# Performance work log

Hardware: AMD Instinct MI355X
Metric: run time of the kernel (lower is better)

Reference implementation:

```python
import jax, jax.numpy as jnp
import numpy as np


def _lstm_encode(x_tbF, W_ih, W_hh, b_ih, b_hh):
    """torch nn.LSTM (single layer), x: [T, B, F]. Returns final (h, c), each [B, H]."""
    H = W_hh.shape[1]
    B = x_tbF.shape[1]
    b = b_ih + b_hh

    def step(carry, xt):
        h, c = carry
        gates = xt @ W_ih.T + h @ W_hh.T + b  # [B, 4H]
        i, f, g, o = jnp.split(gates, 4, axis=-1)
        c = jax.nn.sigmoid(f) * c + jax.nn.sigmoid(i) * jnp.tanh(g)
        h = jax.nn.sigmoid(o) * jnp.tanh(c)
        return (h, c), None

    init = (jnp.zeros((B, H), x_tbF.dtype), jnp.zeros((B, H), x_tbF.dtype))
    (h, c), _ = jax.lax.scan(step, init, x_tbF)
    return h, c


def reference(speed, pos, Ws_ih, Ws_hh, bs_ih, bs_hh, Wp_ih, Wp_hh, bp_ih, bp_hh,
              Wd_ih, Wd_hh, bd_ih, bd_hh, W_fc, b_fc, W_emb, b_emb, seq_len):
    # Encoders consume time-major inputs (module does speed.permute(1,0,2))
    sh, sc = _lstm_encode(jnp.transpose(speed, (1, 0, 2)), Ws_ih, Ws_hh, bs_ih, bs_hh)
    ph, pc = _lstm_encode(jnp.transpose(pos, (1, 0, 2)), Wp_ih, Wp_hh, bp_ih, bp_hh)

    h0 = ph + sh
    c0 = pc + sc
    last_pos0 = pos[:, -1, :]  # [B, 4]
    bd = bd_ih + bd_hh

    def dec_step(carry, _):
        h, c, last_pos = carry
        gates = last_pos @ Wd_ih.T + h @ Wd_hh.T + bd  # [B, 4H]
        i, f, g, o = jnp.split(gates, 4, axis=-1)
        c = jax.nn.sigmoid(f) * c + jax.nn.sigmoid(i) * jnp.tanh(g)
        h = jax.nn.sigmoid(o) * jnp.tanh(c)
        crossing = jax.nn.relu(h @ W_fc.T + b_fc)        # fc_crossing: [B, 2]
        last_pos = jax.nn.relu(crossing @ W_emb.T + b_emb)  # pos_embedding: [B, 4]
        probs = jax.nn.softmax(crossing, axis=1)
        return (h, c, last_pos), probs

    _, probs = jax.lax.scan(dec_step, (h0, c0, last_pos0), None, length=seq_len)
    return jnp.transpose(probs, (1, 0, 2))  # [B, seq_len, 2]


def setup_inputs() -> dict:
    B, T, H, F = 8192, 16, 512, 4
    seq_len = 16
    key = jax.random.key(0)
    ks = jax.random.split(key, 20)
    s = 1.0 / np.sqrt(H)

    def u(k, shape):
        return jax.random.uniform(k, shape, jnp.float32, -s, s)

    return {
        "speed": jax.random.normal(ks[0], (B, T, F), jnp.float32),
        "pos": jax.random.normal(ks[1], (B, T, F), jnp.float32),
        "Ws_ih": u(ks[2], (4 * H, F)), "Ws_hh": u(ks[3], (4 * H, H)),
        "bs_ih": u(ks[4], (4 * H,)), "bs_hh": u(ks[5], (4 * H,)),
        "Wp_ih": u(ks[6], (4 * H, F)), "Wp_hh": u(ks[7], (4 * H, H)),
        "bp_ih": u(ks[8], (4 * H,)), "bp_hh": u(ks[9], (4 * H,)),
        "Wd_ih": u(ks[10], (4 * H, F)), "Wd_hh": u(ks[11], (4 * H, H)),
        "bd_ih": u(ks[12], (4 * H,)), "bd_hh": u(ks[13], (4 * H,)),
        "W_fc": u(ks[14], (2, H)), "b_fc": u(ks[15], (2,)),
        "W_emb": u(ks[16], (4, 2)), "b_emb": u(ks[17], (4,)),
        "seq_len": seq_len,
    }
```

## Files before the change

### kernel.cpp

```cpp
#include <hip/hip_runtime.h>

#define NBLK 256
#define NTHR 512
#define MTILE 32
#define KPADI 592
#define HSTR  528
#define CHB   (9*8*64*16)
#define LSTR  (16*CHB)

typedef __attribute__((ext_vector_type(4))) int int4v;

__device__ inline float ex2(float x){ return __builtin_amdgcn_exp2f(x); }
__device__ inline float rcpf_(float d){ return __builtin_amdgcn_rcpf(d); }
__device__ inline float rcpn(float d){ float r=__builtin_amdgcn_rcpf(d); return r*(2.f-d*r); }
#define LOG2E 1.4426950408889634f
__device__ inline float sigf(float x){ return rcpf_(1.f+ex2(-LOG2E*x)); }
__device__ inline float tanh_(float x){ return 2.f*rcpf_(1.f+ex2(-2.f*LOG2E*x))-1.f; }

__device__ inline void lbar(){
    asm volatile("s_waitcnt lgkmcnt(0)\n\ts_barrier" ::: "memory");
}

__global__ void scale_k(const float* Ws_ih, const float* Ws_hh, const float* bs_ih, const float* bs_hh,
                        const float* Wp_ih, const float* Wp_hh, const float* bp_ih, const float* bp_hh,
                        const float* Wd_ih, const float* Wd_hh, const float* bd_ih, const float* bd_hh,
                        int* smax)
{
    int L = blockIdx.x >> 5;
    int blk = blockIdx.x & 31;
    const float* Wih = L==0 ? Ws_ih : L==1 ? Wp_ih : Wd_ih;
    const float* Whh = L==0 ? Ws_hh : L==1 ? Wp_hh : Wd_hh;
    const float* bih = L==0 ? bs_ih : L==1 ? bp_ih : bd_ih;
    const float* bhh = L==0 ? bs_hh : L==1 ? bp_hh : bd_hh;
    float m = 0.f;
    for (int i = blk*256 + threadIdx.x; i < 2048*512; i += 32*256) m = fmaxf(m, fabsf(Whh[i]));
    for (int i = blk*256 + threadIdx.x; i < 2048*4;   i += 32*256) m = fmaxf(m, fabsf(Wih[i]));
    for (int i = blk*256 + threadIdx.x; i < 2048;     i += 32*256) m = fmaxf(m, 0.5f*fabsf(bih[i]+bhh[i]));
    __shared__ float red[256];
    red[threadIdx.x] = m; __syncthreads();
    for (int s = 128; s; s >>= 1){
        if (threadIdx.x < s) red[threadIdx.x] = fmaxf(red[threadIdx.x], red[threadIdx.x+s]);
        __syncthreads();
    }
    if (threadIdx.x == 0) atomicMax(&smax[L], __float_as_int(red[0]));
}

__global__ void pack_k(const float* Wih, const float* Whh, const float* bih, const float* bhh,
                       const int* smax, int L, unsigned char* dst, float* gsout)
{
    int f4 = blockIdx.x*256 + threadIdx.x;
    if (f4*4 >= LSTR) return;
    float mx = __int_as_float(smax[L]);
    float inv = 127.f / mx;
    if (blockIdx.x==0 && threadIdx.x==0) gsout[L] = mx * (1.f/(127.f*127.f));
    int fb = f4*4;
    int lane=(fb>>4)&63, nt=(fb>>10)&7, t=fb>>13;
    int kt=t%9, chunk=t/9;
    int n = (chunk*8+nt)*16 + (lane&15);
    int ch=n>>7, g=(n>>5)&3, u=n&31;
    int row = g*512 + ch*32 + u;
    int kbase = kt*64 + ((lane>>4)<<4) + (fb&15);
    unsigned out = 0;
    #pragma unroll
    for (int b=0;b<4;++b){
        int k = kbase + b;
        float v = 0.f;
        if (k < 512)      v = Whh[row*512+k];
        else if (k < 528) v = Wih[row*4 + (k&3)];
        else if (k < 530) v = 0.5f*(bih[row]+bhh[row]);
        int q = (int)rintf(v*inv);
        q = q>127?127:(q<-127?-127:q);
        out |= ((unsigned)(q & 255)) << (8*b);
    }
    *(unsigned*)(dst + fb) = out;
}

__global__ __launch_bounds__(NTHR, 1)
void lstm_all(const float* __restrict__ speed, const float* __restrict__ pos,
              const unsigned char* __restrict__ wpack, const float* __restrict__ gsb,
              const float* __restrict__ wfc, const float* __restrict__ bfc,
              const float* __restrict__ wemb, const float* __restrict__ bemb,
              float* __restrict__ out)
{
    __shared__ __align__(16) unsigned char abuf[2][MTILE][KPADI];
    __shared__ __align__(16) unsigned char hsave[MTILE][HSTR];
    __shared__ float csave[MTILE][512];
    __shared__ float smallw[1040];
    __shared__ float partial[NTHR];

    const int tid  = threadIdx.x;
    const int lane = tid & 63;
    const int wv   = tid >> 6;
    const int row0 = blockIdx.x * MTILE;
    const int l15  = lane & 15;
    const int lq   = lane >> 4;
    const int cstag = blockIdx.x & 15;

    const float gs0 = gsb[0], gs1 = gsb[1], gs2 = gsb[2];

    {
        for (int i = tid; i < 2*MTILE*(KPADI/16); i += NTHR) {
            int b = i / (MTILE*(KPADI/16));
            int rmd = i % (MTILE*(KPADI/16));
            int m = rmd / (KPADI/16), c16 = (rmd % (KPADI/16))*16;
            *(int4v*)&abuf[b][m][c16] = (int4v){0,0,0,0};
        }
        for (int i = tid; i < 1024; i += NTHR) smallw[i] = wfc[i];
        if (tid < 2) smallw[1024+tid] = bfc[tid];
        if (tid < 8) smallw[1026+tid] = wemb[tid];
        if (tid < 4) smallw[1034+tid] = bemb[tid];
    }
    lbar();
    if (tid < 64) { int b = tid>>5, m = tid&31; abuf[b][m][528] = 127; abuf[b][m][529] = 127; }
    if (tid < 128) {
        int m = tid>>2, f3 = tid&3;
        float x = speed[((size_t)(row0+m)*16 + 0)*4 + f3];
        int q = (int)rintf(fminf(fmaxf(x*31.75f,-127.f),127.f));
        unsigned char qb = (unsigned char)q;
        abuf[0][m][512+f3]=qb; abuf[0][m][516+f3]=qb; abuf[0][m][520+f3]=qb; abuf[0][m][524+f3]=qb;
    }
    lbar();

    float cc0[16], cc1[16];
    #pragma unroll
    for (int i = 0; i < 16; ++i) { cc0[i]=0.f; cc1[i]=0.f; }

    int4v bA[8], bB[8];

    auto epi = [&](int4v (&acc)[2][8], float (&cc)[16], int chunk, int wbuf,
                   float nK1, float nK2){
        #pragma unroll
        for (int mf=0;mf<2;++mf)
            #pragma unroll
            for (int up=0;up<2;++up)
                #pragma unroll
                for (int r=0;r<4;++r){
                    int idx = (mf*2+up)*4 + r;
                    float fi = (float)acc[mf][0+up][r];
                    float ff = (float)acc[mf][2+up][r];
                    float fg = (float)acc[mf][4+up][r];
                    float fo = (float)acc[mf][6+up][r];
                    float si = rcpf_(1.f+ex2(nK1*fi));
                    float sf = rcpf_(1.f+ex2(nK1*ff));
                    float so = rcpf_(1.f+ex2(nK1*fo));
                    float tg = 2.f*rcpf_(1.f+ex2(nK2*fg)) - 1.f;
                    float cn = sf*cc[idx] + si*tg;
                    cc[idx] = cn;
                    float h = so*tanh_(cn);
                    int q = (int)rintf(h*127.f);
                    abuf[wbuf][mf*16+lq*4+r][chunk*32+up*16+l15] = (unsigned char)q;
                }
    };

    auto step2 = [&](int rb, int wbuf, const unsigned char* wl,
                     float (&c0)[16], float (&c1)[16], float gs, int WARM, int PF){
        const int ch0 = (2*wv + 0 + cstag) & 15;
        const int ch1 = (2*wv + 1 + cstag) & 15;
        const unsigned char* bp0 = wl + (size_t)ch0*CHB + lane*16;
        const unsigned char* bp1 = wl + (size_t)ch1*CHB + lane*16;
        const unsigned char* ar0 = &abuf[rb][l15][0];
        const unsigned char* ar1 = &abuf[rb][16+l15][0];
        const float nK1 = -gs*LOG2E, nK2 = -2.f*gs*LOG2E;
        int4v acc[2][8];
        if (!WARM){
            #pragma unroll
            for (int nt=0;nt<8;++nt) bA[nt] = *(const int4v*)(bp0 + nt*1024);
        }
        #pragma unroll
        for (int mf=0;mf<2;++mf)
            #pragma unroll
            for (int nt=0;nt<8;++nt) acc[mf][nt] = (int4v){0,0,0,0};
        #pragma unroll 1
        for (int kt=0; kt<8; kt+=2){
            const unsigned char* p1 = bp0 + (kt+1)*8192;
            #pragma unroll
            for (int nt=0;nt<8;++nt) bB[nt] = *(const int4v*)(p1 + nt*1024);
            int4v a0 = *(const int4v*)(ar0 + kt*64 + lq*16);
            int4v a1 = *(const int4v*)(ar1 + kt*64 + lq*16);
            #pragma unroll
            for (int nt=0;nt<8;++nt){
                acc[0][nt] = __builtin_amdgcn_mfma_i32_16x16x64_i8(a0, bA[nt], acc[0][nt], 0,0,0);
                acc[1][nt] = __builtin_amdgcn_mfma_i32_16x16x64_i8(a1, bA[nt], acc[1][nt], 0,0,0);
            }
            const unsigned char* p2 = bp0 + (kt+2)*8192;
            #pragma unroll
            for (int nt=0;nt<8;++nt) bA[nt] = *(const int4v*)(p2 + nt*1024);
            a0 = *(const int4v*)(ar0 + (kt+1)*64 + lq*16);
            a1 = *(const int4v*)(ar1 + (kt+1)*64 + lq*16);
            #pragma unroll
            for (int nt=0;nt<8;++nt){
                acc[0][nt] = __builtin_amdgcn_mfma_i32_16x16x64_i8(a0, bB[nt], acc[0][nt], 0,0,0);
                acc[1][nt] = __builtin_amdgcn_mfma_i32_16x16x64_i8(a1, bB[nt], acc[1][nt], 0,0,0);
            }
        }
        #pragma unroll
        for (int nt=0;nt<8;++nt) bB[nt] = *(const int4v*)(bp1 + nt*1024);
        {
            int4v a0 = *(const int4v*)(ar0 + 8*64 + lq*16);
            int4v a1 = *(const int4v*)(ar1 + 8*64 + lq*16);
            #pragma unroll
            for (int nt=0;nt<8;++nt){
                acc[0][nt] = __builtin_amdgcn_mfma_i32_16x16x64_i8(a0, bA[nt], acc[0][nt], 0,0,0);
                acc[1][nt] = __builtin_amdgcn_mfma_i32_16x16x64_i8(a1, bA[nt], acc[1][nt], 0,0,0);
            }
        }
        epi(acc, c0, ch0, wbuf, nK1, nK2);
        #pragma unroll
        for (int mf=0;mf<2;++mf)
            #pragma unroll
            for (int nt=0;nt<8;++nt) acc[mf][nt] = (int4v){0,0,0,0};
        #pragma unroll 1
        for (int kt=0; kt<8; kt+=2){
            const unsigned char* p1 = bp1 + (kt+1)*8192;
            #pragma unroll
            for (int nt=0;nt<8;++nt) bA[nt] = *(const int4v*)(p1 + nt*1024);
            int4v a0 = *(const int4v*)(ar0 + kt*64 + lq*16);
            int4v a1 = *(const int4v*)(ar1 + kt*64 + lq*16);
            #pragma unroll
            for (int nt=0;nt<8;++nt){
                acc[0][nt] = __builtin_amdgcn_mfma_i32_16x16x64_i8(a0, bB[nt], acc[0][nt], 0,0,0);
                acc[1][nt] = __builtin_amdgcn_mfma_i32_16x16x64_i8(a1, bB[nt], acc[1][nt], 0,0,0);
            }
            const unsigned char* p2 = bp1 + (kt+2)*8192;
            #pragma unroll
            for (int nt=0;nt<8;++nt) bB[nt] = *(const int4v*)(p2 + nt*1024);
            a0 = *(const int4v*)(ar0 + (kt+1)*64 + lq*16);
            a1 = *(const int4v*)(ar1 + (kt+1)*64 + lq*16);
            #pragma unroll
            for (int nt=0;nt<8;++nt){
                acc[0][nt] = __builtin_amdgcn_mfma_i32_16x16x64_i8(a0, bA[nt], acc[0][nt], 0,0,0);
                acc[1][nt] = __builtin_amdgcn_mfma_i32_16x16x64_i8(a1, bA[nt], acc[1][nt], 0,0,0);
            }
        }
        if (PF){
            #pragma unroll
            for (int nt=0;nt<8;++nt) bA[nt] = *(const int4v*)(bp0 + nt*1024);
        }
        {
            int4v a0 = *(const int4v*)(ar0 + 8*64 + lq*16);
            int4v a1 = *(const int4v*)(ar1 + 8*64 + lq*16);
            #pragma unroll
            for (int nt=0;nt<8;++nt){
                acc[0][nt] = __builtin_amdgcn_mfma_i32_16x16x64_i8(a0, bB[nt], acc[0][nt], 0,0,0);
                acc[1][nt] = __builtin_amdgcn_mfma_i32_16x16x64_i8(a1, bB[nt], acc[1][nt], 0,0,0);
            }
        }
        epi(acc, c1, ch1, wbuf, nK1, nK2);
    };

    auto pass_dual = [&](const unsigned char* wl, int s, float (&cc)[16], float gs, int (&hq)[16]) {
        const int chunk = (2*wv + s + cstag) & 15;
        const unsigned char* bp = wl + (size_t)chunk*CHB + lane*16;
        const unsigned char* ar0 = &abuf[0][l15][0];
        const unsigned char* ar1 = &abuf[0][16+l15][0];
        int4v acc[2][8];
        #pragma unroll
        for (int mf=0;mf<2;++mf)
            #pragma unroll
            for (int nt=0;nt<8;++nt) acc[mf][nt] = (int4v){0,0,0,0};
        #pragma unroll
        for (int nt=0;nt<8;++nt) bA[nt] = *(const int4v*)(bp + nt*1024);
        #pragma unroll 1
        for (int kt=0; kt<8; kt+=2){
            const unsigned char* p1 = bp + (kt+1)*8192;
            #pragma unroll
            for (int nt=0;nt<8;++nt) bB[nt] = *(const int4v*)(p1 + nt*1024);
            int4v a0 = *(const int4v*)(ar0 + kt*64 + lq*16);
            int4v a1 = *(const int4v*)(ar1 + kt*64 + lq*16);
            #pragma unroll
            for (int nt=0;nt<8;++nt){
                acc[0][nt] = __builtin_amdgcn_mfma_i32_16x16x64_i8(a0, bA[nt], acc[0][nt], 0,0,0);
                acc[1][nt] = __builtin_amdgcn_mfma_i32_16x16x64_i8(a1, bA[nt], acc[1][nt], 0,0,0);
            }
            const unsigned char* p2 = bp + (kt+2)*8192;
            #pragma unroll
            for (int nt=0;nt<8;++nt) bA[nt] = *(const int4v*)(p2 + nt*1024);
            a0 = *(const int4v*)(ar0 + (kt+1)*64 + lq*16);
            a1 = *(const int4v*)(ar1 + (kt+1)*64 + lq*16);
            #pragma unroll
            for (int nt=0;nt<8;++nt){
                acc[0][nt] = __builtin_amdgcn_mfma_i32_16x16x64_i8(a0, bB[nt], acc[0][nt], 0,0,0);
                acc[1][nt] = __builtin_amdgcn_mfma_i32_16x16x64_i8(a1, bB[nt], acc[1][nt], 0,0,0);
            }
        }
        {
            int4v a0 = *(const int4v*)(ar0 + 8*64 + lq*16);
            int4v a1 = *(const int4v*)(ar1 + 8*64 + lq*16);
            #pragma unroll
            for (int nt=0;nt<8;++nt){
                acc[0][nt] = __builtin_amdgcn_mfma_i32_16x16x64_i8(a0, bA[nt], acc[0][nt], 0,0,0);
                acc[1][nt] = __builtin_amdgcn_mfma_i32_16x16x64_i8(a1, bA[nt], acc[1][nt], 0,0,0);
            }
        }
        {
            const unsigned char* hr0 = &hsave[l15][0];
            const unsigned char* hr1 = &hsave[16+l15][0];
            #pragma unroll
            for (int nt=0;nt<8;++nt) bA[nt] = *(const int4v*)(bp + nt*1024);
            #pragma unroll 1
            for (int kt=0; kt<8; kt+=2){
                const unsigned char* p1 = bp + (kt+1)*8192;
                #pragma unroll
                for (int nt=0;nt<8;++nt) bB[nt] = *(const int4v*)(p1 + nt*1024);
                int4v a0 = *(const int4v*)(hr0 + kt*64 + lq*16);
                int4v a1 = *(const int4v*)(hr1 + kt*64 + lq*16);
                #pragma unroll
                for (int nt=0;nt<8;++nt){
                    acc[0][nt] = __builtin_amdgcn_mfma_i32_16x16x64_i8(a0, bA[nt], acc[0][nt], 0,0,0);
                    acc[1][nt] = __builtin_amdgcn_mfma_i32_16x16x64_i8(a1, bA[nt], acc[1][nt], 0,0,0);
                }
                const unsigned char* p2 = bp + (kt+2)*8192;
                #pragma unroll
                for (int nt=0;nt<8;++nt) bA[nt] = *(const int4v*)(p2 + nt*1024);
                a0 = *(const int4v*)(hr0 + (kt+1)*64 + lq*16);
                a1 = *(const int4v*)(hr1 + (kt+1)*64 + lq*16);
                #pragma unroll
                for (int nt=0;nt<8;++nt){
                    acc[0][nt] = __builtin_amdgcn_mfma_i32_16x16x64_i8(a0, bB[nt], acc[0][nt], 0,0,0);
                    acc[1][nt] = __builtin_amdgcn_mfma_i32_16x16x64_i8(a1, bB[nt], acc[1][nt], 0,0,0);
                }
            }
        }
        #pragma unroll
        for (int mf=0;mf<2;++mf)
            #pragma unroll
            for (int up=0;up<2;++up)
                #pragma unroll
                for (int r=0;r<4;++r){
                    int idx = (mf*2+up)*4 + r;
                    float gi = (float)acc[mf][0+up][r] * gs;
                    float gf = (float)acc[mf][2+up][r] * gs;
                    float gg = (float)acc[mf][4+up][r] * gs;
                    float go = (float)acc[mf][6+up][r] * gs;
                    float cn = sigf(gf)*cc[idx] + sigf(gi)*tanh_(gg);
                    cc[idx] = cn;
                    float h = sigf(go)*tanh_(cn);
                    hq[idx] = (int)rintf(h*127.f);
                }
    };

    const unsigned char* wsp = wpack;
    const unsigned char* wpp = wpack + (size_t)LSTR;
    const unsigned char* wdp = wpack + 2*(size_t)LSTR;

    #pragma unroll 1
    for (int t=0;t<16;++t){
        int rb=t&1, wbuf=(t+1)&1;
        if (t<15 && tid<128){
            int m=tid>>2, f3=tid&3;
            float x = speed[((size_t)(row0+m)*16 + t+1)*4 + f3];
            int q = (int)rintf(fminf(fmaxf(x*31.75f,-127.f),127.f));
            unsigned char qb=(unsigned char)q;
            abuf[wbuf][m][512+f3]=qb; abuf[wbuf][m][516+f3]=qb; abuf[wbuf][m][520+f3]=qb; abuf[wbuf][m][524+f3]=qb;
        }
        step2(rb,wbuf,wsp,cc0,cc1,gs0, (t>0), (t<15));
        lbar();
    }
    for (int i=tid; i<MTILE*32; i+=NTHR){
        int m=i>>5, cb=(i&31)*16;
        *(int4v*)&hsave[m][cb] = *(const int4v*)&abuf[0][m][cb];
        *(int4v*)&abuf[0][m][cb] = (int4v){0,0,0,0};
    }
    #pragma unroll
    for (int s2=0;s2<2;++s2)
        #pragma unroll
        for (int mf=0;mf<2;++mf)
            #pragma unroll
            for (int up=0;up<2;++up)
                #pragma unroll
                for (int r=0;r<4;++r){
                    int idx=(mf*2+up)*4+r;
                    int ch=(2*wv+s2+cstag)&15;
                    csave[mf*16+lq*4+r][ch*32+up*16+l15] = s2 ? cc1[idx] : cc0[idx];
                }
    #pragma unroll
    for (int i=0;i<16;++i){ cc0[i]=0.f; cc1[i]=0.f; }
    if (tid < 128) {
        int m = tid>>2, f3 = tid&3;
        float x = pos[((size_t)(row0+m)*16 + 0)*4 + f3];
        int q = (int)rintf(fminf(fmaxf(x*31.75f,-127.f),127.f));
        unsigned char qb = (unsigned char)q;
        abuf[0][m][512+f3]=qb; abuf[0][m][516+f3]=qb; abuf[0][m][520+f3]=qb; abuf[0][m][524+f3]=qb;
    }
    lbar();

    #pragma unroll 1
    for (int t=0;t<16;++t){
        int rb=t&1, wbuf=(t+1)&1;
        if (t<15 && tid<128){
            int m=tid>>2, f3=tid&3;
            float x = pos[((size_t)(row0+m)*16 + t+1)*4 + f3];
            int q = (int)rintf(fminf(fmaxf(x*31.75f,-127.f),127.f));
            unsigned char qb=(unsigned char)q;
            abuf[wbuf][m][512+f3]=qb; abuf[wbuf][m][516+f3]=qb; abuf[wbuf][m][520+f3]=qb; abuf[wbuf][m][524+f3]=qb;
        }
        step2(rb,wbuf,wpp,cc0,cc1,gs1, (t>0), (t<15));
        lbar();
    }
    if (tid < 128) {
        int m = tid>>2, f3 = tid&3;
        float x = pos[((size_t)(row0+m)*16 + 15)*4 + f3];
        int q = (int)rintf(fminf(fmaxf(x*31.75f,-127.f),127.f));
        unsigned char qb = (unsigned char)q;
        abuf[0][m][512+f3]=qb; abuf[0][m][516+f3]=qb; abuf[0][m][520+f3]=qb; abuf[0][m][524+f3]=qb;
    }
    #pragma unroll
    for (int s2=0;s2<2;++s2)
        #pragma unroll
        for (int mf=0;mf<2;++mf)
            #pragma unroll
            for (int up=0;up<2;++up)
                #pragma unroll
                for (int r=0;r<4;++r){
                    int idx=(mf*2+up)*4+r;
                    int ch=(2*wv+s2+cstag)&15;
                    float v = csave[mf*16+lq*4+r][ch*32+up*16+l15];
                    if (s2) cc1[idx]+=v; else cc0[idx]+=v;
                }
    lbar();

    #pragma unroll 1
    for (int t=0;t<16;++t){
        int hb;
        if (t == 0) {
            int hq0[16], hq1[16];
            pass_dual(wdp, 0, cc0, gs2, hq0);
            pass_dual(wdp, 1, cc1, gs2, hq1);
            lbar();
            #pragma unroll
            for (int s2=0;s2<2;++s2)
                #pragma unroll
                for (int mf=0;mf<2;++mf)
                    #pragma unroll
                    for (int up=0;up<2;++up)
                        #pragma unroll
                        for (int r=0;r<4;++r){
                            int idx=(mf*2+up)*4+r;
                            int ch=(2*wv+s2+cstag)&15;
                            int q = s2 ? hq1[idx] : hq0[idx];
                            abuf[0][mf*16+lq*4+r][ch*32+up*16+l15] = (unsigned char)q;
                        }
            hb = 0;
        } else {
            int rb=(t+1)&1, wbuf=t&1;
            step2(rb,wbuf,wdp,cc0,cc1,gs2, (t>1), (t<15));
            hb = wbuf;
        }
        lbar();
        {
            int r = lane>>1, col = lane&1;
            const unsigned char* hp = &abuf[hb][r][wv*64];
            const float* wp = &smallw[col*512 + wv*64];
            float p = 0.f;
            #pragma unroll
            for (int k4=0;k4<16;++k4){
                int v = *(const int*)(hp + k4*4);
                p += (float)((signed char)(v    )) * wp[k4*4+0];
                p += (float)((signed char)(v>>8 )) * wp[k4*4+1];
                p += (float)((signed char)(v>>16)) * wp[k4*4+2];
                p += (float)((signed char)(v>>24)) * wp[k4*4+3];
            }
            partial[wv*64 + lane] = p;
        }
        lbar();
        if (wv == 0) {
            float p = 0.f;
            #pragma unroll
            for (int i=0;i<8;++i) p += partial[i*64 + lane];
            int r = lane>>1, col = lane&1;
            p = p*(1.f/127.f) + smallw[1024+col];
            float cr = fmaxf(p, 0.f);
            float other = __shfl_xor(cr, 1, 64);
            float mx = fmaxf(cr, other);
            float e0 = ex2(LOG2E*(cr-mx)), e1 = ex2(LOG2E*(other-mx));
            out[((size_t)(row0+r))*32 + t*2 + col] = e0*rcpn(e0+e1);
            float c0v = col ? other : cr;
            float c1v = col ? cr : other;
            #pragma unroll
            for (int q2=0;q2<2;++q2){
                int e = col*2 + q2;
                float lp = fmaxf(c0v*smallw[1026+e*2] + c1v*smallw[1026+e*2+1] + smallw[1034+e], 0.f);
                int qv = (int)rintf(fminf(lp*31.75f, 127.f));
                unsigned char qb = (unsigned char)qv;
                abuf[hb][r][512+e]=qb; abuf[hb][r][516+e]=qb; abuf[hb][r][520+e]=qb; abuf[hb][r][524+e]=qb;
            }
        }
        lbar();
    }
}

extern "C" void kernel_launch(void* const* d_in, const int* in_sizes, int n_in,
                              void* d_out, int out_size, void* d_ws, size_t ws_size,
                              hipStream_t stream)
{
    (void)in_sizes; (void)n_in; (void)out_size; (void)ws_size;
    const float* speed = (const float*)d_in[0];
    const float* pos   = (const float*)d_in[1];
    const float* Ws_ih = (const float*)d_in[2];
    const float* Ws_hh = (const float*)d_in[3];
    const float* bs_ih = (const float*)d_in[4];
    const float* bs_hh = (const float*)d_in[5];
    const float* Wp_ih = (const float*)d_in[6];
    const float* Wp_hh = (const float*)d_in[7];
    const float* bp_ih = (const float*)d_in[8];
    const float* bp_hh = (const float*)d_in[9];
    const float* Wd_ih = (const float*)d_in[10];
    const float* Wd_hh = (const float*)d_in[11];
    const float* bd_ih = (const float*)d_in[12];
    const float* bd_hh = (const float*)d_in[13];
    const float* W_fc  = (const float*)d_in[14];
    const float* b_fc  = (const float*)d_in[15];
    const float* W_emb = (const float*)d_in[16];
    const float* b_emb = (const float*)d_in[17];

    unsigned char* wp8 = (unsigned char*)d_ws;
    int*   smax  = (int*)(wp8 + 3*(size_t)LSTR);
    float* gsout = (float*)(wp8 + 3*(size_t)LSTR + 16);

    scale_k<<<96, 256, 0, stream>>>(Ws_ih,Ws_hh,bs_ih,bs_hh, Wp_ih,Wp_hh,bp_ih,bp_hh,
                                    Wd_ih,Wd_hh,bd_ih,bd_hh, smax);
    int gb = (LSTR/4 + 255) / 256;
    pack_k<<<gb, 256, 0, stream>>>(Ws_ih, Ws_hh, bs_ih, bs_hh, smax, 0, wp8,                  gsout);
    pack_k<<<gb, 256, 0, stream>>>(Wp_ih, Wp_hh, bp_ih, bp_hh, smax, 1, wp8 +   (size_t)LSTR, gsout);
    pack_k<<<gb, 256, 0, stream>>>(Wd_ih, Wd_hh, bd_ih, bd_hh, smax, 2, wp8 + 2*(size_t)LSTR, gsout);
    lstm_all<<<NBLK, NTHR, 0, stream>>>(speed, pos, wp8, gsout,
                                        W_fc, b_fc, W_emb, b_emb, (float*)d_out);
}
```

Measured before the change: 772.7 us.

## Double-buffer weight prefetch two k-tiles ahead across chunks and phases

Restructures the int8 MFMA k-loop so two B-fragment register sets are always in flight, prefetching two k-tiles ahead and carrying the first two tiles of the next chunk, next timestep, or next LSTM phase across epilogues and barriers. The dual pass in the decoder's first step is rewritten with the same macros so its weight loads stay pipelined. The aim is to hide global-memory latency for weight fetches at chunk boundaries. It adds register pressure and more complex cross-phase pointer bookkeeping.

```diff
diff --git a/kernel.cpp b/kernel.cpp
--- a/kernel.cpp
+++ b/kernel.cpp
@@ -20,6 +20,130 @@
 __device__ inline void lbar(){
     asm volatile("s_waitcnt lgkmcnt(0)\n\ts_barrier" ::: "memory");
 }
+
+#define CHUNK9(BX, BY, AR0, AR1, BP, NXB)                                                   \
+    _Pragma("unroll 1")                                                                     \
+    for (int kt=0; kt<6; kt+=2){                                                            \
+        int4v a0 = *(const int4v*)((AR0) + kt*64 + lq*16);                                  \
+        int4v a1 = *(const int4v*)((AR1) + kt*64 + lq*16);                                  \
+        _Pragma("unroll")                                                                   \
+        for (int nt=0;nt<8;++nt){                                                           \
+            acc[0][nt] = __builtin_amdgcn_mfma_i32_16x16x64_i8(a0, BX[nt], acc[0][nt], 0,0,0); \
+            acc[1][nt] = __builtin_amdgcn_mfma_i32_16x16x64_i8(a1, BX[nt], acc[1][nt], 0,0,0); \
+        }                                                                                   \
+        { const unsigned char* p2 = (BP) + (kt+2)*8192;                                     \
+          _Pragma("unroll")                                                                 \
+          for (int nt=0;nt<8;++nt) BX[nt] = *(const int4v*)(p2 + nt*1024); }                \
+        a0 = *(const int4v*)((AR0) + (kt+1)*64 + lq*16);                                    \
+        a1 = *(const int4v*)((AR1) + (kt+1)*64 + lq*16);                                    \
+        _Pragma("unroll")                                                                   \
+        for (int nt=0;nt<8;++nt){                                                           \
+            acc[0][nt] = __builtin_amdgcn_mfma_i32_16x16x64_i8(a0, BY[nt], acc[0][nt], 0,0,0); \
+            acc[1][nt] = __builtin_amdgcn_mfma_i32_16x16x64_i8(a1, BY[nt], acc[1][nt], 0,0,0); \
+        }                                                                                   \
+        { const unsigned char* p3 = (BP) + (kt+3)*8192;                                     \
+          _Pragma("unroll")                                                                 \
+          for (int nt=0;nt<8;++nt) BY[nt] = *(const int4v*)(p3 + nt*1024); }                \
+    }                                                                                       \
+    {         \
+        int4v a0 = *(const int4v*)((AR0) + 6*64 + lq*16);                                   \
+        int4v a1 = *(const int4v*)((AR1) + 6*64 + lq*16);                                   \
+        _Pragma("unroll")                                                                   \
+        for (int nt=0;nt<8;++nt){                                                           \
+            acc[0][nt] = __builtin_amdgcn_mfma_i32_16x16x64_i8(a0, BX[nt], acc[0][nt], 0,0,0); \
+            acc[1][nt] = __builtin_amdgcn_mfma_i32_16x16x64_i8(a1, BX[nt], acc[1][nt], 0,0,0); \
+        }                                                                                   \
+        { const unsigned char* p8 = (BP) + 8*8192;                                          \
+          _Pragma("unroll")                                                                 \
+          for (int nt=0;nt<8;++nt) BX[nt] = *(const int4v*)(p8 + nt*1024); }                \
+        a0 = *(const int4v*)((AR0) + 7*64 + lq*16);                                         \
+        a1 = *(const int4v*)((AR1) + 7*64 + lq*16);                                         \
+        _Pragma("unroll")                                                                   \
+        for (int nt=0;nt<8;++nt){                                                           \
+            acc[0][nt] = __builtin_amdgcn_mfma_i32_16x16x64_i8(a0, BY[nt], acc[0][nt], 0,0,0); \
+            acc[1][nt] = __builtin_amdgcn_mfma_i32_16x16x64_i8(a1, BY[nt], acc[1][nt], 0,0,0); \
+        }                                                                                   \
+        _Pragma("unroll")                                                                   \
+        for (int nt=0;nt<8;++nt) BY[nt] = *(const int4v*)((NXB) + nt*1024);                 \
+    }                                                                                       \
+    {                                           \
+        int4v a0 = *(const int4v*)((AR0) + 8*64 + lq*16);                                   \
+        int4v a1 = *(const int4v*)((AR1) + 8*64 + lq*16);                                   \
+        _Pragma("unroll")                                                                   \
+        for (int nt=0;nt<8;++nt){                                                           \
+            acc[0][nt] = __builtin_amdgcn_mfma_i32_16x16x64_i8(a0, BX[nt], acc[0][nt], 0,0,0); \
+            acc[1][nt] = __builtin_amdgcn_mfma_i32_16x16x64_i8(a1, BX[nt], acc[1][nt], 0,0,0); \
+        }                                                                                   \
+        _Pragma("unroll")                                                                   \
+        for (int nt=0;nt<8;++nt) BX[nt] = *(const int4v*)((NXB) + 8192 + nt*1024);          \
+    }
+
+#define CHUNK8(BX, BY, AR0, AR1, BP, NXB)                                                   \
+    _Pragma("unroll 1")                                                                     \
+    for (int kt=0; kt<4; kt+=2){                                                            \
+        int4v a0 = *(const int4v*)((AR0) + kt*64 + lq*16);                                  \
+        int4v a1 = *(const int4v*)((AR1) + kt*64 + lq*16);                                  \
+        _Pragma("unroll")                                                                   \
+        for (int nt=0;nt<8;++nt){                                                           \
+            acc[0][nt] = __builtin_amdgcn_mfma_i32_16x16x64_i8(a0, BX[nt], acc[0][nt], 0,0,0); \
+            acc[1][nt] = __builtin_amdgcn_mfma_i32_16x16x64_i8(a1, BX[nt], acc[1][nt], 0,0,0); \
+        }                                                                                   \
+        { const unsigned char* p2 = (BP) + (kt+2)*8192;                                     \
+          _Pragma("unroll")                                                                 \
+          for (int nt=0;nt<8;++nt) BX[nt] = *(const int4v*)(p2 + nt*1024); }                \
+        a0 = *(const int4v*)((AR0) + (kt+1)*64 + lq*16);                                    \
+        a1 = *(const int4v*)((AR1) + (kt+1)*64 + lq*16);                                    \
+        _Pragma("unroll")                                                                   \
+        for (int nt=0;nt<8;++nt){                                                           \
+            acc[0][nt] = __builtin_amdgcn_mfma_i32_16x16x64_i8(a0, BY[nt], acc[0][nt], 0,0,0); \
+            acc[1][nt] = __builtin_amdgcn_mfma_i32_16x16x64_i8(a1, BY[nt], acc[1][nt], 0,0,0); \
+        }                                                                                   \
+        { const unsigned char* p3 = (BP) + (kt+3)*8192;                                     \
+          _Pragma("unroll")                                                                 \
+          for (int nt=0;nt<8;++nt) BY[nt] = *(const int4v*)(p3 + nt*1024); }                \
+    }                                                                                       \
+    {                   \
+        int4v a0 = *(const int4v*)((AR0) + 4*64 + lq*16);                                   \
+        int4v a1 = *(const int4v*)((AR1) + 4*64 + lq*16);                                   \
+        _Pragma("unroll")                                                                   \
+        for (int nt=0;nt<8;++nt){                                                           \
+            acc[0][nt] = __builtin_amdgcn_mfma_i32_16x16x64_i8(a0, BX[nt], acc[0][nt], 0,0,0); \
+            acc[1][nt] = __builtin_amdgcn_mfma_i32_16x16x64_i8(a1, BX[nt], acc[1][nt], 0,0,0); \
+        }                                                                                   \
+        { const unsigned char* p2 = (BP) + 6*8192;                                          \
+          _Pragma("unroll")                                                                 \
+          for (int nt=0;nt<8;++nt) BX[nt] = *(const int4v*)(p2 + nt*1024); }                \
+        a0 = *(const int4v*)((AR0) + 5*64 + lq*16);                                         \
+        a1 = *(const int4v*)((AR1) + 5*64 + lq*16);                                         \
+        _Pragma("unroll")                                                                   \
+        for (int nt=0;nt<8;++nt){                                                           \
+            acc[0][nt] = __builtin_amdgcn_mfma_i32_16x16x64_i8(a0, BY[nt], acc[0][nt], 0,0,0); \
+            acc[1][nt] = __builtin_amdgcn_mfma_i32_16x16x64_i8(a1, BY[nt], acc[1][nt], 0,0,0); \
+        }                                                                                   \
+        { const unsigned char* p3 = (BP) + 7*8192;                                          \
+          _Pragma("unroll")                                                                 \
+          for (int nt=0;nt<8;++nt) BY[nt] = *(const int4v*)(p3 + nt*1024); }                \
+    }                                                                                       \
+    {    \
+        int4v a0 = *(const int4v*)((AR0) + 6*64 + lq*16);                                   \
+        int4v a1 = *(const int4v*)((AR1) + 6*64 + lq*16);                                   \
+        _Pragma("unroll")                                                                   \
+        for (int nt=0;nt<8;++nt){                                                           \
+            acc[0][nt] = __builtin_amdgcn_mfma_i32_16x16x64_i8(a0, BX[nt], acc[0][nt], 0,0,0); \
+            acc[1][nt] = __builtin_amdgcn_mfma_i32_16x16x64_i8(a1, BX[nt], acc[1][nt], 0,0,0); \
+        }                                                                                   \
+        _Pragma("unroll")                                                                   \
+        for (int nt=0;nt<8;++nt) BX[nt] = *(const int4v*)((NXB) + nt*1024);                 \
+        a0 = *(const int4v*)((AR0) + 7*64 + lq*16);                                         \
+        a1 = *(const int4v*)((AR1) + 7*64 + lq*16);                                         \
+        _Pragma("unroll")                                                                   \
+        for (int nt=0;nt<8;++nt){                                                           \
+            acc[0][nt] = __builtin_amdgcn_mfma_i32_16x16x64_i8(a0, BY[nt], acc[0][nt], 0,0,0); \
+            acc[1][nt] = __builtin_amdgcn_mfma_i32_16x16x64_i8(a1, BY[nt], acc[1][nt], 0,0,0); \
+        }                                                                                   \
+        _Pragma("unroll")                                                                   \
+        for (int nt=0;nt<8;++nt) BY[nt] = *(const int4v*)((NXB) + 8192 + nt*1024);          \
+    }
 
 __global__ void scale_k(const float* Ws_ih, const float* Ws_hh, const float* bs_ih, const float* bs_hh,
                         const float* Wp_ih, const float* Wp_hh, const float* bp_ih, const float* bp_hh,
@@ -95,8 +219,26 @@
     const int l15  = lane & 15;
     const int lq   = lane >> 4;
     const int cstag = blockIdx.x & 15;
+    const int ch0 = (2*wv + 0 + cstag) & 15;
+    const int ch1 = (2*wv + 1 + cstag) & 15;
 
     const float gs0 = gsb[0], gs1 = gsb[1], gs2 = gsb[2];
+
+    const unsigned char* wsp = wpack;
+    const unsigned char* wpp = wpack + (size_t)LSTR;
+    const unsigned char* wdp = wpack + 2*(size_t)LSTR;
+    const unsigned char* sp0 = wsp + (size_t)ch0*CHB + lane*16;
+    const unsigned char* sp1 = wsp + (size_t)ch1*CHB + lane*16;
+    const unsigned char* pp0 = wpp + (size_t)ch0*CHB + lane*16;
+    const unsigned char* pp1 = wpp + (size_t)ch1*CHB + lane*16;
+    const unsigned char* dp0 = wdp + (size_t)ch0*CHB + lane*16;
+    const unsigned char* dp1 = wdp + (size_t)ch1*CHB + lane*16;
+
+    int4v bA[8], bB[8];
+    #pragma unroll
+    for (int nt=0;nt<8;++nt) bA[nt] = *(const int4v*)(sp0 + nt*1024);
+    #pragma unroll
+    for (int nt=0;nt<8;++nt) bB[nt] = *(const int4v*)(sp0 + 8192 + nt*1024);
 
     {
         for (int i = tid; i < 2*MTILE*(KPADI/16); i += NTHR) {
@@ -124,8 +266,6 @@
     float cc0[16], cc1[16];
     #pragma unroll
     for (int i = 0; i < 16; ++i) { cc0[i]=0.f; cc1[i]=0.f; }
-
-    int4v bA[8], bB[8];
 
     auto epi = [&](int4v (&acc)[2][8], float (&cc)[16], int chunk, int wbuf,
                    float nK1, float nK2){
@@ -152,175 +292,28 @@
                 }
     };
 
-    auto step2 = [&](int rb, int wbuf, const unsigned char* wl,
-                     float (&c0)[16], float (&c1)[16], float gs, int WARM, int PF){
-        const int ch0 = (2*wv + 0 + cstag) & 15;
-        const int ch1 = (2*wv + 1 + cstag) & 15;
-        const unsigned char* bp0 = wl + (size_t)ch0*CHB + lane*16;
-        const unsigned char* bp1 = wl + (size_t)ch1*CHB + lane*16;
+    auto step2 = [&](int rb, int wbuf, const unsigned char* bp0, const unsigned char* bp1,
+                     const unsigned char* np0,
+                     float (&c0)[16], float (&c1)[16], float gs){
         const unsigned char* ar0 = &abuf[rb][l15][0];
         const unsigned char* ar1 = &abuf[rb][16+l15][0];
         const float nK1 = -gs*LOG2E, nK2 = -2.f*gs*LOG2E;
         int4v acc[2][8];
-        if (!WARM){
-            #pragma unroll
-            for (int nt=0;nt<8;++nt) bA[nt] = *(const int4v*)(bp0 + nt*1024);
-        }
         #pragma unroll
         for (int mf=0;mf<2;++mf)
             #pragma unroll
             for (int nt=0;nt<8;++nt) acc[mf][nt] = (int4v){0,0,0,0};
-        #pragma unroll 1
-        for (int kt=0; kt<8; kt+=2){
-            const unsigned char* p1 = bp0 + (kt+1)*8192;
-            #pragma unroll
-            for (int nt=0;nt<8;++nt) bB[nt] = *(const int4v*)(p1 + nt*1024);
-            int4v a0 = *(const int4v*)(ar0 + kt*64 + lq*16);
-            int4v a1 = *(const int4v*)(ar1 + kt*64 + lq*16);
-            #pragma unroll
-            for (int nt=0;nt<8;++nt){
-                acc[0][nt] = __builtin_amdgcn_mfma_i32_16x16x64_i8(a0, bA[nt], acc[0][nt], 0,0,0);
-                acc[1][nt] = __builtin_amdgcn_mfma_i32_16x16x64_i8(a1, bA[nt], acc[1][nt], 0,0,0);
-            }
-            const unsigned char* p2 = bp0 + (kt+2)*8192;
-            #pragma unroll
-            for (int nt=0;nt<8;++nt) bA[nt] = *(const int4v*)(p2 + nt*1024);
-            a0 = *(const int4v*)(ar0 + (kt+1)*64 + lq*16);
-            a1 = *(const int4v*)(ar1 + (kt+1)*64 + lq*16);
-            #pragma unroll
-            for (int nt=0;nt<8;++nt){
-                acc[0][nt] = __builtin_amdgcn_mfma_i32_16x16x64_i8(a0, bB[nt], acc[0][nt], 0,0,0);
-                acc[1][nt] = __builtin_amdgcn_mfma_i32_16x16x64_i8(a1, bB[nt], acc[1][nt], 0,0,0);
-            }
-        }
-        #pragma unroll
-        for (int nt=0;nt<8;++nt) bB[nt] = *(const int4v*)(bp1 + nt*1024);
-        {
-            int4v a0 = *(const int4v*)(ar0 + 8*64 + lq*16);
-            int4v a1 = *(const int4v*)(ar1 + 8*64 + lq*16);
-            #pragma unroll
-            for (int nt=0;nt<8;++nt){
-                acc[0][nt] = __builtin_amdgcn_mfma_i32_16x16x64_i8(a0, bA[nt], acc[0][nt], 0,0,0);
-                acc[1][nt] = __builtin_amdgcn_mfma_i32_16x16x64_i8(a1, bA[nt], acc[1][nt], 0,0,0);
-            }
-        }
+        CHUNK9(bA, bB, ar0, ar1, bp0, bp1)
         epi(acc, c0, ch0, wbuf, nK1, nK2);
         #pragma unroll
         for (int mf=0;mf<2;++mf)
             #pragma unroll
             for (int nt=0;nt<8;++nt) acc[mf][nt] = (int4v){0,0,0,0};
-        #pragma unroll 1
-        for (int kt=0; kt<8; kt+=2){
-            const unsigned char* p1 = bp1 + (kt+1)*8192;
-            #pragma unroll
-            for (int nt=0;nt<8;++nt) bA[nt] = *(const int4v*)(p1 + nt*1024);
-            int4v a0 = *(const int4v*)(ar0 + kt*64 + lq*16);
-            int4v a1 = *(const int4v*)(ar1 + kt*64 + lq*16);
-            #pragma unroll
-            for (int nt=0;nt<8;++nt){
-                acc[0][nt] = __builtin_amdgcn_mfma_i32_16x16x64_i8(a0, bB[nt], acc[0][nt], 0,0,0);
-                acc[1][nt] = __builtin_amdgcn_mfma_i32_16x16x64_i8(a1, bB[nt], acc[1][nt], 0,0,0);
-            }
-            const unsigned char* p2 = bp1 + (kt+2)*8192;
-            #pragma unroll
-            for (int nt=0;nt<8;++nt) bB[nt] = *(const int4v*)(p2 + nt*1024);
-            a0 = *(const int4v*)(ar0 + (kt+1)*64 + lq*16);
-            a1 = *(const int4v*)(ar1 + (kt+1)*64 + lq*16);
-            #pragma unroll
-            for (int nt=0;nt<8;++nt){
-                acc[0][nt] = __builtin_amdgcn_mfma_i32_16x16x64_i8(a0, bA[nt], acc[0][nt], 0,0,0);
-                acc[1][nt] = __builtin_amdgcn_mfma_i32_16x16x64_i8(a1, bA[nt], acc[1][nt], 0,0,0);
-            }
-        }
-        if (PF){
-            #pragma unroll
-            for (int nt=0;nt<8;++nt) bA[nt] = *(const int4v*)(bp0 + nt*1024);
-        }
-        {
-            int4v a0 = *(const int4v*)(ar0 + 8*64 + lq*16);
-            int4v a1 = *(const int4v*)(ar1 + 8*64 + lq*16);
-            #pragma unroll
-            for (int nt=0;nt<8;++nt){
-                acc[0][nt] = __builtin_amdgcn_mfma_i32_16x16x64_i8(a0, bB[nt], acc[0][nt], 0,0,0);
-                acc[1][nt] = __builtin_amdgcn_mfma_i32_16x16x64_i8(a1, bB[nt], acc[1][nt], 0,0,0);
-            }
-        }
+        CHUNK9(bB, bA, ar0, ar1, bp1, np0)
         epi(acc, c1, ch1, wbuf, nK1, nK2);
     };
 
-    auto pass_dual = [&](const unsigned char* wl, int s, float (&cc)[16], float gs, int (&hq)[16]) {
-        const int chunk = (2*wv + s + cstag) & 15;
-        const unsigned char* bp = wl + (size_t)chunk*CHB + lane*16;
-        const unsigned char* ar0 = &abuf[0][l15][0];
-        const unsigned char* ar1 = &abuf[0][16+l15][0];
-        int4v acc[2][8];
-        #pragma unroll
-        for (int mf=0;mf<2;++mf)
-            #pragma unroll
-            for (int nt=0;nt<8;++nt) acc[mf][nt] = (int4v){0,0,0,0};
-        #pragma unroll
-        for (int nt=0;nt<8;++nt) bA[nt] = *(const int4v*)(bp + nt*1024);
-        #pragma unroll 1
-        for (int kt=0; kt<8; kt+=2){
-            const unsigned char* p1 = bp + (kt+1)*8192;
-            #pragma unroll
-            for (int nt=0;nt<8;++nt) bB[nt] = *(const int4v*)(p1 + nt*1024);
-            int4v a0 = *(const int4v*)(ar0 + kt*64 + lq*16);
-            int4v a1 = *(const int4v*)(ar1 + kt*64 + lq*16);
-            #pragma unroll
-            for (int nt=0;nt<8;++nt){
-                acc[0][nt] = __builtin_amdgcn_mfma_i32_16x16x64_i8(a0, bA[nt], acc[0][nt], 0,0,0);
-                acc[1][nt] = __builtin_amdgcn_mfma_i32_16x16x64_i8(a1, bA[nt], acc[1][nt], 0,0,0);
-            }
-            const unsigned char* p2 = bp + (kt+2)*8192;
-            #pragma unroll
-            for (int nt=0;nt<8;++nt) bA[nt] = *(const int4v*)(p2 + nt*1024);
-            a0 = *(const int4v*)(ar0 + (kt+1)*64 + lq*16);
-            a1 = *(const int4v*)(ar1 + (kt+1)*64 + lq*16);
-            #pragma unroll
-            for (int nt=0;nt<8;++nt){
-                acc[0][nt] = __builtin_amdgcn_mfma_i32_16x16x64_i8(a0, bB[nt], acc[0][nt], 0,0,0);
-                acc[1][nt] = __builtin_amdgcn_mfma_i32_16x16x64_i8(a1, bB[nt], acc[1][nt], 0,0,0);
-            }
-        }
-        {
-            int4v a0 = *(const int4v*)(ar0 + 8*64 + lq*16);
-            int4v a1 = *(const int4v*)(ar1 + 8*64 + lq*16);
-            #pragma unroll
-            for (int nt=0;nt<8;++nt){
-                acc[0][nt] = __builtin_amdgcn_mfma_i32_16x16x64_i8(a0, bA[nt], acc[0][nt], 0,0,0);
-                acc[1][nt] = __builtin_amdgcn_mfma_i32_16x16x64_i8(a1, bA[nt], acc[1][nt], 0,0,0);
-            }
-        }
-        {
-            const unsigned char* hr0 = &hsave[l15][0];
-            const unsigned char* hr1 = &hsave[16+l15][0];
-            #pragma unroll
-            for (int nt=0;nt<8;++nt) bA[nt] = *(const int4v*)(bp + nt*1024);
-            #pragma unroll 1
-            for (int kt=0; kt<8; kt+=2){
-                const unsigned char* p1 = bp + (kt+1)*8192;
-                #pragma unroll
-                for (int nt=0;nt<8;++nt) bB[nt] = *(const int4v*)(p1 + nt*1024);
-                int4v a0 = *(const int4v*)(hr0 + kt*64 + lq*16);
-                int4v a1 = *(const int4v*)(hr1 + kt*64 + lq*16);
-                #pragma unroll
-                for (int nt=0;nt<8;++nt){
-                    acc[0][nt] = __builtin_amdgcn_mfma_i32_16x16x64_i8(a0, bA[nt], acc[0][nt], 0,0,0);
-                    acc[1][nt] = __builtin_amdgcn_mfma_i32_16x16x64_i8(a1, bA[nt], acc[1][nt], 0,0,0);
-                }
-                const unsigned char* p2 = bp + (kt+2)*8192;
-                #pragma unroll
-                for (int nt=0;nt<8;++nt) bA[nt] = *(const int4v*)(p2 + nt*1024);
-                a0 = *(const int4v*)(hr0 + (kt+1)*64 + lq*16);
-                a1 = *(const int4v*)(hr1 + (kt+1)*64 + lq*16);
-                #pragma unroll
-                for (int nt=0;nt<8;++nt){
-                    acc[0][nt] = __builtin_amdgcn_mfma_i32_16x16x64_i8(a0, bB[nt], acc[0][nt], 0,0,0);
-                    acc[1][nt] = __builtin_amdgcn_mfma_i32_16x16x64_i8(a1, bB[nt], acc[1][nt], 0,0,0);
-                }
-            }
-        }
+    auto pd_epi = [&](int4v (&acc)[2][8], float (&cc)[16], float gs, int (&hq)[16]){
         #pragma unroll
         for (int mf=0;mf<2;++mf)
             #pragma unroll
@@ -339,10 +332,6 @@
                 }
     };
 
-    const unsigned char* wsp = wpack;
-    const unsigned char* wpp = wpack + (size_t)LSTR;
-    const unsigned char* wdp = wpack + 2*(size_t)LSTR;
-
     #pragma unroll 1
     for (int t=0;t<16;++t){
         int rb=t&1, wbuf=(t+1)&1;
@@ -353,7 +342,7 @@
             unsigned char qb=(unsigned char)q;
             abuf[wbuf][m][512+f3]=qb; abuf[wbuf][m][516+f3]=qb; abuf[wbuf][m][520+f3]=qb; abuf[wbuf][m][524+f3]=qb;
         }
-        step2(rb,wbuf,wsp,cc0,cc1,gs0, (t>0), (t<15));
+        step2(rb,wbuf, sp0, sp1, (t<15)? sp0 : pp0, cc0, cc1, gs0);
         lbar();
     }
     for (int i=tid; i<MTILE*32; i+=NTHR){
@@ -394,7 +383,7 @@
             unsigned char qb=(unsigned char)q;
             abuf[wbuf][m][512+f3]=qb; abuf[wbuf][m][516+f3]=qb; abuf[wbuf][m][520+f3]=qb; abuf[wbuf][m][524+f3]=qb;
         }
-        step2(rb,wbuf,wpp,cc0,cc1,gs1, (t>0), (t<15));
+        step2(rb,wbuf, pp0, pp1, (t<15)? pp0 : dp0, cc0, cc1, gs1);
         lbar();
     }
     if (tid < 128) {
@@ -424,8 +413,25 @@
         int hb;
         if (t == 0) {
             int hq0[16], hq1[16];
-            pass_dual(wdp, 0, cc0, gs2, hq0);
-            pass_dual(wdp, 1, cc1, gs2, hq1);
+            const unsigned char* ar0 = &abuf[0][l15][0];
+            const unsigned char* ar1 = &abuf[0][16+l15][0];
+            const unsigned char* hr0 = &hsave[l15][0];
+            const unsigned char* hr1 = &hsave[16+l15][0];
+            int4v acc[2][8];
+            #pragma unroll
+            for (int mf=0;mf<2;++mf)
+                #pragma unroll
+                for (int nt=0;nt<8;++nt) acc[mf][nt] = (int4v){0,0,0,0};
+            CHUNK9(bA, bB, ar0, ar1, dp0, dp0)
+            CHUNK8(bB, bA, hr0, hr1, dp0, dp1)
+            pd_epi(acc, cc0, gs2, hq0);
+            #pragma unroll
+            for (int mf=0;mf<2;++mf)
+                #pragma unroll
+                for (int nt=0;nt<8;++nt) acc[mf][nt] = (int4v){0,0,0,0};
+            CHUNK9(bB, bA, ar0, ar1, dp1, dp1)
+            CHUNK8(bA, bB, hr0, hr1, dp1, dp0)
+            pd_epi(acc, cc1, gs2, hq1);
             lbar();
             #pragma unroll
             for (int s2=0;s2<2;++s2)
@@ -443,7 +449,7 @@
             hb = 0;
         } else {
             int rb=(t+1)&1, wbuf=t&1;
-            step2(rb,wbuf,wdp,cc0,cc1,gs2, (t>1), (t<15));
+            step2(rb,wbuf, dp0, dp1, dp0, cc0, cc1, gs2);
             hb = wbuf;
         }
         lbar();
```

After: 1.131 ms. 46.3% more time.
